# Optimization experiments

Hardware: AMD Instinct MI355X
Metric: run time of the kernel (lower is better)

Reference implementation:

```python
import jax, jax.numpy as jnp
import numpy as np

B, S = 16, 512
IN_DIM, ATTN_DIM, DEPTH, HEADS, DH = 512, 512, 4, 8, 64
CB_DIM, CB_SIZE, MAX_SEQ = 64, 8192, 544


def _ln(x, g, b):
    mu = x.mean(-1, keepdims=True)
    v = ((x - mu) ** 2).mean(-1, keepdims=True)
    return (x - mu) / jnp.sqrt(v + 1e-5) * g + b


def setup_inputs() -> dict:
    key = jax.random.key(0)
    ks = jax.random.split(key, 16)
    sc = 0.02
    d = {
        "x": jax.random.normal(ks[0], (B, S, IN_DIM), jnp.float32),
        "w_in": jax.random.normal(ks[1], (IN_DIM, ATTN_DIM), jnp.float32) * sc,
        "b_in": jnp.zeros((ATTN_DIM,), jnp.float32),
        "pos_emb": jax.random.normal(ks[2], (MAX_SEQ, ATTN_DIM), jnp.float32) * sc,
        "ln1_g": jnp.ones((DEPTH, ATTN_DIM), jnp.float32),
        "ln1_b": jnp.zeros((DEPTH, ATTN_DIM), jnp.float32),
        "wq": jax.random.normal(ks[3], (DEPTH, ATTN_DIM, ATTN_DIM), jnp.float32) * sc,
        "wk": jax.random.normal(ks[4], (DEPTH, ATTN_DIM, ATTN_DIM), jnp.float32) * sc,
        "wv": jax.random.normal(ks[5], (DEPTH, ATTN_DIM, ATTN_DIM), jnp.float32) * sc,
        "wo": jax.random.normal(ks[6], (DEPTH, ATTN_DIM, ATTN_DIM), jnp.float32) * sc,
        "ln2_g": jnp.ones((DEPTH, ATTN_DIM), jnp.float32),
        "ln2_b": jnp.zeros((DEPTH, ATTN_DIM), jnp.float32),
        "ff_w1": jax.random.normal(ks[7], (DEPTH, ATTN_DIM, 4 * ATTN_DIM), jnp.float32) * sc,
        "ff_b1": jnp.zeros((DEPTH, 4 * ATTN_DIM), jnp.float32),
        "ff_w2": jax.random.normal(ks[8], (DEPTH, 4 * ATTN_DIM, ATTN_DIM), jnp.float32) * sc,
        "ff_b2": jnp.zeros((DEPTH, ATTN_DIM), jnp.float32),
        "lnf_g": jnp.ones((ATTN_DIM,), jnp.float32),
        "lnf_b": jnp.zeros((ATTN_DIM,), jnp.float32),
        "w_out": jax.random.normal(ks[9], (ATTN_DIM, CB_DIM), jnp.float32) * sc,
        "b_out": jnp.zeros((CB_DIM,), jnp.float32),
        "codebook": jax.random.normal(ks[10], (CB_SIZE, CB_DIM), jnp.float32),
    }
    return d


def _attn(h, wq, wk, wv, wo):
    b, s, _ = h.shape
    q = jnp.einsum('bsd,de->bse', h, wq).reshape(b, s, HEADS, DH)
    k = jnp.einsum('bsd,de->bse', h, wk).reshape(b, s, HEADS, DH)
    v = jnp.einsum('bsd,de->bse', h, wv).reshape(b, s, HEADS, DH)
    scores = jnp.einsum('bqhd,bkhd->bhqk', q, k) * (DH ** -0.5)
    a = jax.nn.softmax(scores, axis=-1)
    o = jnp.einsum('bhqk,bkhd->bqhd', a, v).reshape(b, s, ATTN_DIM)
    return jnp.einsum('bse,ed->bsd', o, wo)


def reference(x, w_in, b_in, pos_emb, ln1_g, ln1_b, wq, wk, wv, wo,
              ln2_g, ln2_b, ff_w1, ff_b1, ff_w2, ff_b2, lnf_g, lnf_b,
              w_out, b_out, codebook):
    s = x.shape[1]
    # ContinuousTransformerWrapper: project in + absolute pos emb
    h = jnp.einsum('bsd,de->bse', x, w_in) + b_in + pos_emb[:s]
    # pre-norm encoder layers: attn + ff, each residual
    for i in range(DEPTH):
        h = h + _attn(_ln(h, ln1_g[i], ln1_b[i]), wq[i], wk[i], wv[i], wo[i])
        g = _ln(h, ln2_g[i], ln2_b[i])
        g = jax.nn.gelu(jnp.einsum('bsd,df->bsf', g, ff_w1[i]) + ff_b1[i])
        h = h + jnp.einsum('bsf,fd->bsd', g, ff_w2[i]) + ff_b2[i]
    h = _ln(h, lnf_g, lnf_b)
    z = jnp.einsum('bsd,dc->bsc', h, w_out) + b_out  # [B,S,CB_DIM]
    # VectorQuantize: euclidean nearest codebook entry
    d2 = (z ** 2).sum(-1, keepdims=True) - 2.0 * jnp.einsum('bsc,kc->bsk', z, codebook) \
         + (codebook ** 2).sum(-1)  # [B,S,CB_SIZE]
    idx = jnp.argmin(d2, axis=-1)
    q = codebook[idx]  # [B,S,CB_DIM]
    commit_loss = jnp.mean((jax.lax.stop_gradient(q) - z) ** 2)  # commitment_weight=1.0
    q_st = z + jax.lax.stop_gradient(q - z)  # straight-through
    return q_st.sum(axis=1), commit_loss
```

## Files before the change

kernel.cpp:

```cpp
#include <hip/hip_runtime.h>
#include <cmath>

#define BATCH 16
#define SEQ 512
#define DMODEL 512
#define NDEPTH 4
#define NHEADS 8
#define DHEAD 64
#define DFF 2048
#define CBD 64
#define CBS 8192
#define MROWS (BATCH * SEQ)

typedef unsigned short u16;
typedef __attribute__((ext_vector_type(8))) short short8;
typedef __attribute__((ext_vector_type(4))) float f32x4;
typedef __attribute__((ext_vector_type(4))) unsigned short u16x4;

__device__ __forceinline__ u16 f2bf(float f) {
    unsigned u = __float_as_uint(f);
    u += 0x7fff + ((u >> 16) & 1);
    return (u16)(u >> 16);
}
__device__ __forceinline__ float bf2f(u16 h) {
    return __uint_as_float(((unsigned)h) << 16);
}

__device__ __forceinline__ void async16(u16* lds, const u16* g) {
    __builtin_amdgcn_global_load_lds(
        (const __attribute__((address_space(1))) unsigned int*)g,
        (__attribute__((address_space(3))) unsigned int*)lds, 16, 0, 0);
}

__device__ __forceinline__ float gelu_tanh(float u) {
    float t = fmaf(0.07135481627f * u, u * u, 1.5957691216f * u);
    return u / (1.0f + __expf(-t));
}

__global__ void zero_kernel(float* __restrict__ p, int n) {
    int i = blockIdx.x * 256 + threadIdx.x;
    if (i < n) p[i] = 0.0f;
}

__global__ void cbn_kernel(const float* __restrict__ cb, float* __restrict__ cbn) {
    int c = blockIdx.x * 256 + threadIdx.x;
    if (c >= CBS) return;
    const float* row = cb + (size_t)c * CBD;
    float s = 0.0f;
#pragma unroll
    for (int d = 0; d < CBD; ++d) s += row[d] * row[d];
    cbn[c] = s;
}

__global__ __launch_bounds__(256) void wtrans_kernel(
    const float* __restrict__ W, u16* __restrict__ Th, u16* __restrict__ Tl,
    int K, int N, long inLS, long outLS) {
    __shared__ float t[32][33];
    const float* Ws = W + (size_t)blockIdx.z * inLS;
    u16* Tho = Th + (size_t)blockIdx.z * outLS;
    u16* Tlo = Tl + (size_t)blockIdx.z * outLS;
    int n0 = blockIdx.x * 32, k0 = blockIdx.y * 32;
    int tx = threadIdx.x & 31, ty = threadIdx.x >> 5;
#pragma unroll
    for (int r = ty; r < 32; r += 8) t[r][tx] = Ws[(size_t)(k0 + r) * N + n0 + tx];
    __syncthreads();
#pragma unroll
    for (int r = ty; r < 32; r += 8) {
        float v = t[tx][r];
        size_t o = (size_t)(n0 + r) * K + k0 + tx;
        u16 hh = f2bf(v);
        Tho[o] = hh;
        Tlo[o] = f2bf(v - bf2f(hh));
    }
}

__global__ __launch_bounds__(256) void vtrans_kernel(
    const u16* __restrict__ Qh, const u16* __restrict__ Ql,
    u16* __restrict__ VTh, u16* __restrict__ VTl) {
    __shared__ u16 t[64][68];
    int s0 = blockIdx.x * 64;
    int hh = blockIdx.y;
    int b = blockIdx.z & 15, plane = blockIdx.z >> 4;
    const u16* src = (plane ? Ql : Qh) + ((size_t)(16 + hh) * MROWS) * 64;
    u16* dst = (plane ? VTl : VTh);
    int tid = threadIdx.x;
    int rr = tid >> 4, c4 = (tid & 15) * 4;
#pragma unroll
    for (int i = 0; i < 4; ++i) {
        int r = rr + i * 16;
        const u16* p = src + (size_t)(b * SEQ + s0 + r) * 64 + c4;
        *(u16x4*)(&t[r][c4]) = *(const u16x4*)p;
    }
    __syncthreads();
#pragma unroll
    for (int i = 0; i < 4; ++i) {
        int r = rr + i * 16;
        u16x4 v;
        v.x = t[c4 + 0][r]; v.y = t[c4 + 1][r]; v.z = t[c4 + 2][r]; v.w = t[c4 + 3][r];
        *(u16x4*)(dst + (size_t)b * SEQ * DMODEL + (size_t)(hh * 64 + r) * SEQ + s0 + c4) = v;
    }
}

__global__ void split_kernel(const float* __restrict__ X, u16* __restrict__ H,
                             u16* __restrict__ L, int n) {
    int i = blockIdx.x * 256 + threadIdx.x;
    if (i < n) {
        float v = X[i];
        u16 hh = f2bf(v);
        H[i] = hh;
        L[i] = f2bf(v - bf2f(hh));
    }
}

__global__ __launch_bounds__(256) void ln_kernel(
    const float* __restrict__ X,
    const float* __restrict__ C0, const float* __restrict__ C1,
    const float* __restrict__ bias2, const float* __restrict__ pos2,
    float* __restrict__ Xout,
    float* __restrict__ Y, u16* __restrict__ Yh, u16* __restrict__ Yl,
    const float* __restrict__ g, const float* __restrict__ b) {
    int row  = blockIdx.x * 4 + (threadIdx.x >> 6);
    int lane = threadIdx.x & 63;
    float v[8];
    float s = 0.0f;
#pragma unroll
    for (int j = 0; j < 8; ++j) {
        int d = lane + j * 64;
        size_t o = (size_t)row * DMODEL + d;
        float t = X ? X[o] : 0.0f;
        if (C0)    t += C0[o] + C1[o];
        if (bias2) t += bias2[d];
        if (pos2)  t += pos2[(size_t)(row & (SEQ - 1)) * DMODEL + d];
        v[j] = t;
        if (Xout) Xout[o] = t;
        s += t;
    }
#pragma unroll
    for (int off = 32; off; off >>= 1) s += __shfl_xor(s, off);
    float mu  = s * (1.0f / DMODEL);
    float var = 0.0f;
#pragma unroll
    for (int j = 0; j < 8; ++j) { float d = v[j] - mu; var += d * d; }
#pragma unroll
    for (int off = 32; off; off >>= 1) var += __shfl_xor(var, off);
    float r = rsqrtf(var * (1.0f / DMODEL) + 1e-5f);
#pragma unroll
    for (int j = 0; j < 8; ++j) {
        int d = lane + j * 64;
        float y = (v[j] - mu) * r * g[d] + b[d];
        size_t o = (size_t)row * DMODEL + d;
        if (Y) Y[o] = y;
        if (Yh) {
            u16 hh = f2bf(y);
            Yh[o] = hh;
            Yl[o] = f2bf(y - bf2f(hh));
        }
    }
}

__global__ __launch_bounds__(256) void gemm3_kernel(
    const u16* __restrict__ Ah, const u16* __restrict__ Al,
    const u16* __restrict__ Bh, const u16* __restrict__ Bl,
    float* __restrict__ Cf, u16* __restrict__ Ch, u16* __restrict__ Cl,
    const float* __restrict__ bias, const float* __restrict__ res,
    const float* __restrict__ pos, int M, int N, int K, int gelu,
    float* __restrict__ Cs0, float* __restrict__ Cs1, int kslice, int qkvscatter) {
    __shared__ __align__(16) u16 AsH[128 * 64];
    __shared__ __align__(16) u16 AsL[128 * 64];
    __shared__ __align__(16) u16 BsH[128 * 64];
    __shared__ __align__(16) u16 BsL[128 * 64];

    int tid  = threadIdx.x;
    int w    = tid >> 6, lane = tid & 63;
    int wr   = w >> 1, wc = w & 1;
    int quad = lane >> 4, l16 = lane & 15;
    int m0   = blockIdx.x * 128;
    int n0   = blockIdx.y * 128;
    int ksA  = (kslice > 0) ? blockIdx.z * kslice : 0;
    int ksB  = (kslice > 0) ? ksA + kslice : K;

    f32x4 acc[4][4];
#pragma unroll
    for (int i = 0; i < 4; ++i)
#pragma unroll
        for (int j = 0; j < 4; ++j) acc[i][j] = (f32x4){0.f, 0.f, 0.f, 0.f};

    int ldsoff[4];
    size_t goff[4];
#pragma unroll
    for (int r = 0; r < 4; ++r) {
        int cidx = tid + 256 * r;
        int row = cidx >> 3;
        int cg = (cidx & 7) ^ (row & 7);
        ldsoff[r] = cidx * 8;
        goff[r] = (size_t)row * K + cg * 8;
    }

    const u16* AbaseH = Ah + (size_t)m0 * K;
    const u16* AbaseL = Al + (size_t)m0 * K;
    const u16* BbaseH = Bh + (size_t)n0 * K;
    const u16* BbaseL = Bl + (size_t)n0 * K;

    for (int ks = ksA; ks < ksB; ks += 64) {
        __syncthreads();
#pragma unroll
        for (int r = 0; r < 4; ++r) {
            size_t g = goff[r] + ks;
            async16(&AsH[ldsoff[r]], AbaseH + g);
            async16(&AsL[ldsoff[r]], AbaseL + g);
            async16(&BsH[ldsoff[r]], BbaseH + g);
            async16(&BsL[ldsoff[r]], BbaseL + g);
        }
        __syncthreads();
#pragma unroll
        for (int s = 0; s < 2; ++s) {
            short8 afh[4], afl[4];
#pragma unroll
            for (int i = 0; i < 4; ++i) {
                int row = wr * 64 + i * 16 + l16;
                int off = row * 64 + (((s << 2) | quad) ^ (row & 7)) * 8;
                afh[i] = *(const short8*)&AsH[off];
                afl[i] = *(const short8*)&AsL[off];
            }
#pragma unroll
            for (int j = 0; j < 4; ++j) {
                int rowb = wc * 64 + j * 16 + l16;
                int offb = rowb * 64 + (((s << 2) | quad) ^ (rowb & 7)) * 8;
                short8 bh = *(const short8*)&BsH[offb];
                short8 bl = *(const short8*)&BsL[offb];
#pragma unroll
                for (int i = 0; i < 4; ++i) {
                    acc[i][j] = __builtin_amdgcn_mfma_f32_16x16x32_bf16(afh[i], bh, acc[i][j], 0, 0, 0);
                    acc[i][j] = __builtin_amdgcn_mfma_f32_16x16x32_bf16(afl[i], bh, acc[i][j], 0, 0, 0);
                    acc[i][j] = __builtin_amdgcn_mfma_f32_16x16x32_bf16(afh[i], bl, acc[i][j], 0, 0, 0);
                }
            }
        }
    }

    float* Cspl = (kslice > 0) ? (blockIdx.z ? Cs1 : Cs0) : nullptr;
    int mbase = m0 + wr * 64;
    int nbase = n0 + wc * 64;
#pragma unroll
    for (int mi = 0; mi < 4; ++mi)
#pragma unroll
        for (int ni = 0; ni < 4; ++ni) {
            f32x4 a = acc[mi][ni];
#pragma unroll
            for (int r = 0; r < 4; ++r) {
                int m = mbase + mi * 16 + quad * 4 + r;
                int n = nbase + ni * 16 + l16;
                float v = a[r];
                size_t o = qkvscatter
                    ? ((size_t)(n >> 6) * M + m) * 64 + (n & 63)
                    : (size_t)m * N + n;
                if (Cspl) { Cspl[o] = v; continue; }
                if (bias) v += bias[n];
                if (pos)  v += pos[(size_t)(m & (SEQ - 1)) * N + n];
                if (res)  v += res[(size_t)m * N + n];
                if (gelu) v = gelu_tanh(v);
                if (Cf) Cf[o] = v;
                if (Ch) {
                    u16 hh = f2bf(v);
                    Ch[o] = hh;
                    Cl[o] = f2bf(v - bf2f(hh));
                }
            }
        }
}

__global__ __launch_bounds__(256) void gemm_kernel(
    const float* __restrict__ A, const float* __restrict__ Bm,
    float* __restrict__ C, const float* __restrict__ bias,
    int M, int N, int K) {
    __shared__ float As[16][68];
    __shared__ float Bs[16][64];
    int tid = threadIdx.x;
    int tx = tid & 15, ty = tid >> 4;
    int a_m = tid >> 2, a_k = (tid & 3) * 4;
    int b_k = tid >> 4, b_n = (tid & 15) * 4;
    const float* Arow = A + (size_t)(blockIdx.x * 64 + a_m) * K;
    const float* Bcol = Bm + (size_t)blockIdx.y * 64 + b_n;
    float acc[4][4] = {};
    for (int k0 = 0; k0 < K; k0 += 16) {
        float4 av = *(const float4*)(Arow + k0 + a_k);
        float4 bv = *(const float4*)(Bcol + (size_t)(k0 + b_k) * N);
        __syncthreads();
        As[a_k + 0][a_m] = av.x; As[a_k + 1][a_m] = av.y;
        As[a_k + 2][a_m] = av.z; As[a_k + 3][a_m] = av.w;
        *(float4*)(&Bs[b_k][b_n]) = bv;
        __syncthreads();
#pragma unroll
        for (int kk = 0; kk < 16; ++kk) {
            float4 a4 = *(const float4*)(&As[kk][ty * 4]);
            float4 b4 = *(const float4*)(&Bs[kk][tx * 4]);
            float ar[4] = {a4.x, a4.y, a4.z, a4.w};
            float br[4] = {b4.x, b4.y, b4.z, b4.w};
#pragma unroll
            for (int i = 0; i < 4; ++i)
#pragma unroll
                for (int j = 0; j < 4; ++j) acc[i][j] = fmaf(ar[i], br[j], acc[i][j]);
        }
    }
    int m0 = blockIdx.x * 64 + ty * 4;
    int n0 = blockIdx.y * 64 + tx * 4;
#pragma unroll
    for (int i = 0; i < 4; ++i) {
        float vv[4];
#pragma unroll
        for (int j = 0; j < 4; ++j) {
            float t = acc[i][j];
            if (bias) t += bias[n0 + j];
            vv[j] = t;
        }
        *(float4*)(C + (size_t)(m0 + i) * N + n0) = make_float4(vv[0], vv[1], vv[2], vv[3]);
    }
}

__global__ __launch_bounds__(256) void attn_flash_kernel(
    const u16* __restrict__ QKh, const u16* __restrict__ QKl,
    const u16* __restrict__ VTh, const u16* __restrict__ VTl,
    u16* __restrict__ Oh, u16* __restrict__ Ol) {
    int bh = blockIdx.x & 127;
    int qt = blockIdx.x >> 7;
    int bb = bh >> 3, hh = bh & 7;

    __shared__ __align__(16) float Pw[4][16 * 68];

    int tid = threadIdx.x;
    int w = tid >> 6, lane = tid & 63;
    int quad = lane >> 4, l16 = lane & 15;
    int qtile = qt * 4 + w;
    float* P = Pw[w];

    const u16* qrh = QKh + ((size_t)hh * MROWS + bb * SEQ + qtile * 16 + l16) * 64 + quad * 8;
    const u16* qrl = QKl + ((size_t)hh * MROWS + bb * SEQ + qtile * 16 + l16) * 64 + quad * 8;
    short8 Qh0 = *(const short8*)qrh;
    short8 Qh1 = *(const short8*)(qrh + 32);
    short8 Ql0 = *(const short8*)qrl;
    short8 Ql1 = *(const short8*)(qrl + 32);

    float lsum[4] = {0.f, 0.f, 0.f, 0.f};
    f32x4 acc[4];
#pragma unroll
    for (int dt = 0; dt < 4; ++dt) acc[dt] = (f32x4){0.f, 0.f, 0.f, 0.f};

    const u16* KbH = QKh + ((size_t)(8 + hh) * MROWS + bb * SEQ) * 64;
    const u16* KbL = QKl + ((size_t)(8 + hh) * MROWS + bb * SEQ) * 64;
    const u16* VbH = VTh + (size_t)bb * SEQ * DMODEL + (size_t)(hh * 64) * SEQ;
    const u16* VbL = VTl + (size_t)bb * SEQ * DMODEL + (size_t)(hh * 64) * SEQ;

    for (int kt = 0; kt < 8; ++kt) {
        int kb = kt * 64;
#pragma unroll
        for (int s = 0; s < 4; ++s) {
            const u16* kh = KbH + (size_t)(kb + s * 16 + l16) * 64 + quad * 8;
            const u16* kl = KbL + (size_t)(kb + s * 16 + l16) * 64 + quad * 8;
            f32x4 a = (f32x4){0.f, 0.f, 0.f, 0.f};
            {
                short8 Kh0 = *(const short8*)kh;
                short8 Kh1 = *(const short8*)(kh + 32);
                a = __builtin_amdgcn_mfma_f32_16x16x32_bf16(Qh0, Kh0, a, 0, 0, 0);
                a = __builtin_amdgcn_mfma_f32_16x16x32_bf16(Qh1, Kh1, a, 0, 0, 0);
                a = __builtin_amdgcn_mfma_f32_16x16x32_bf16(Ql0, Kh0, a, 0, 0, 0);
                a = __builtin_amdgcn_mfma_f32_16x16x32_bf16(Ql1, Kh1, a, 0, 0, 0);
            }
            {
                short8 Kl0 = *(const short8*)kl;
                short8 Kl1 = *(const short8*)(kl + 32);
                a = __builtin_amdgcn_mfma_f32_16x16x32_bf16(Qh0, Kl0, a, 0, 0, 0);
                a = __builtin_amdgcn_mfma_f32_16x16x32_bf16(Qh1, Kl1, a, 0, 0, 0);
            }
#pragma unroll
            for (int r = 0; r < 4; ++r) {
                float p = __expf(a[r] * 0.125f);
                lsum[r] += p;
                P[(quad * 4 + r) * 68 + s * 16 + l16] = p;
            }
        }
#pragma unroll
        for (int ks = 0; ks < 2; ++ks) {
            short8 ph, pl;
            {
                const float* src = &P[l16 * 68 + ks * 32 + quad * 8];
                f32x4 a0 = *(const f32x4*)src;
                f32x4 a1 = *(const f32x4*)(src + 4);
                float v[8] = {a0[0], a0[1], a0[2], a0[3], a1[0], a1[1], a1[2], a1[3]};
#pragma unroll
                for (int j = 0; j < 8; ++j) {
                    u16 hv = f2bf(v[j]);
                    ph[j] = (short)hv;
                    pl[j] = (short)f2bf(v[j] - bf2f(hv));
                }
            }
#pragma unroll
            for (int dt = 0; dt < 4; ++dt) {
                const u16* vh = VbH + (size_t)(dt * 16 + l16) * SEQ + kb + ks * 32 + quad * 8;
                const u16* vl = VbL + (size_t)(dt * 16 + l16) * SEQ + kb + ks * 32 + quad * 8;
                short8 Vh = *(const short8*)vh;
                short8 Vl = *(const short8*)vl;
                acc[dt] = __builtin_amdgcn_mfma_f32_16x16x32_bf16(ph, Vh, acc[dt], 0, 0, 0);
                acc[dt] = __builtin_amdgcn_mfma_f32_16x16x32_bf16(pl, Vh, acc[dt], 0, 0, 0);
                acc[dt] = __builtin_amdgcn_mfma_f32_16x16x32_bf16(ph, Vl, acc[dt], 0, 0, 0);
            }
        }
    }

#pragma unroll
    for (int r = 0; r < 4; ++r) {
#pragma unroll
        for (int off = 8; off; off >>= 1) lsum[r] += __shfl_xor(lsum[r], off);
    }
#pragma unroll
    for (int r = 0; r < 4; ++r) {
        float inv = 1.0f / lsum[r];
        size_t rowoff = (size_t)(bb * SEQ + qtile * 16 + quad * 4 + r) * DMODEL + hh * 64;
#pragma unroll
        for (int dt = 0; dt < 4; ++dt) {
            float v = acc[dt][r] * inv;
            u16 hv = f2bf(v);
            Oh[rowoff + dt * 16 + l16] = hv;
            Ol[rowoff + dt * 16 + l16] = f2bf(v - bf2f(hv));
        }
    }
}

__global__ __launch_bounds__(256) void vq3_kernel(
    const float* __restrict__ Z, const u16* __restrict__ Zh, const u16* __restrict__ Zl,
    const u16* __restrict__ CBh, const u16* __restrict__ CBl,
    const float* __restrict__ CB, const float* __restrict__ CBN,
    float* __restrict__ out) {
    __shared__ float sbest[4][16];
    __shared__ int sidx[4][16];
    __shared__ int ibest[16];
    __shared__ float psum[4][64];
    __shared__ float cl4[4];

    int tid = threadIdx.x;
    int w = tid >> 6, lane = tid & 63;
    int quad = lane >> 4, l16 = lane & 15;
    int row0 = blockIdx.x * 16;

    const u16* zph = Zh + (size_t)(row0 + l16) * CBD + quad * 8;
    const u16* zpl = Zl + (size_t)(row0 + l16) * CBD + quad * 8;
    short8 Z0h = *(const short8*)zph;
    short8 Z1h = *(const short8*)(zph + 32);
    short8 Z0l = *(const short8*)zpl;
    short8 Z1l = *(const short8*)(zpl + 32);

    float best[4] = {3.4e38f, 3.4e38f, 3.4e38f, 3.4e38f};
    int bidx[4] = {0, 0, 0, 0};

    short8 A0h, A1h, A0l, A1l;  float An;
    short8 B0h, B1h, B0l, B1l;  float Bn;
    short8 C0h, C1h, C0l, C1l;  float Cn;
    short8 D0h, D1h, D0l, D1l;  float Dn;

#define LOADB(bk, cc) {                                            \
    int c_ = (cc);                                                 \
    const u16* ph_ = CBh + (size_t)c_ * CBD + quad * 8;            \
    const u16* pl_ = CBl + (size_t)c_ * CBD + quad * 8;            \
    bk##0h = *(const short8*)ph_;  bk##1h = *(const short8*)(ph_ + 32); \
    bk##0l = *(const short8*)pl_;  bk##1l = *(const short8*)(pl_ + 32); \
    bk##n  = CBN[c_]; }

#define COMPB(bk, cc) {                                                          \
    f32x4 a_ = (f32x4){0.f, 0.f, 0.f, 0.f};                                      \
    int c_ = (cc);                                                               \
    a_ = __builtin_amdgcn_mfma_f32_16x16x32_bf16(Z0h, bk##0h, a_, 0, 0, 0);      \
    a_ = __builtin_amdgcn_mfma_f32_16x16x32_bf16(Z1h, bk##1h, a_, 0, 0, 0);      \
    a_ = __builtin_amdgcn_mfma_f32_16x16x32_bf16(Z0l, bk##0h, a_, 0, 0, 0);      \
    a_ = __builtin_amdgcn_mfma_f32_16x16x32_bf16(Z1l, bk##1h, a_, 0, 0, 0);      \
    a_ = __builtin_amdgcn_mfma_f32_16x16x32_bf16(Z0h, bk##0l, a_, 0, 0, 0);      \
    a_ = __builtin_amdgcn_mfma_f32_16x16x32_bf16(Z1h, bk##1l, a_, 0, 0, 0);      \
    _Pragma("unroll")                                                            \
    for (int r = 0; r < 4; ++r) {                                                \
        float s_ = bk##n - 2.0f * a_[r];                                         \
        if (s_ < best[r]) { best[r] = s_; bidx[r] = c_; }                        \
    } }

    const int NW = CBS / 4;
    int cbase = w * NW;
    LOADB(A, cbase + l16);
    LOADB(B, cbase + 16 + l16);
    LOADB(C, cbase + 32 + l16);
    LOADB(D, cbase + 48 + l16);
    for (int t = 0; t < NW; t += 64) {
        COMPB(A, cbase + t + l16);       LOADB(A, cbase + ((t + 64)  & (NW - 1)) + l16);
        COMPB(B, cbase + t + 16 + l16);  LOADB(B, cbase + ((t + 80)  & (NW - 1)) + l16);
        COMPB(C, cbase + t + 32 + l16);  LOADB(C, cbase + ((t + 96)  & (NW - 1)) + l16);
        COMPB(D, cbase + t + 48 + l16);  LOADB(D, cbase + ((t + 112) & (NW - 1)) + l16);
    }

#undef LOADB
#undef COMPB

#pragma unroll
    for (int off = 8; off; off >>= 1) {
#pragma unroll
        for (int r = 0; r < 4; ++r) {
            float ov = __shfl_xor(best[r], off);
            int oi = __shfl_xor(bidx[r], off);
            if (ov < best[r] || (ov == best[r] && oi < bidx[r])) { best[r] = ov; bidx[r] = oi; }
        }
    }
    if (l16 == 0) {
#pragma unroll
        for (int r = 0; r < 4; ++r) {
            sbest[w][quad * 4 + r] = best[r];
            sidx[w][quad * 4 + r] = bidx[r];
        }
    }
    __syncthreads();
    if (tid < 16) {
        float bv = sbest[0][tid];
        int bi = sidx[0][tid];
#pragma unroll
        for (int ww = 1; ww < 4; ++ww) {
            float ov = sbest[ww][tid];
            int oi = sidx[ww][tid];
            if (ov < bv || (ov == bv && oi < bi)) { bv = ov; bi = oi; }
        }
        ibest[tid] = bi;
    }
    __syncthreads();

    int d2 = lane;
    float qacc = 0.0f, closs = 0.0f;
#pragma unroll
    for (int j = 0; j < 4; ++j) {
        int r2 = w * 4 + j;
        int bi = ibest[r2];
        float q = CB[(size_t)bi * CBD + d2];
        float z = Z[(size_t)(row0 + r2) * CBD + d2];
        qacc += q;
        float df = q - z;
        closs += df * df;
    }
    psum[w][d2] = qacc;
#pragma unroll
    for (int off = 32; off; off >>= 1) closs += __shfl_xor(closs, off);
    if (d2 == 0) cl4[w] = closs;
    __syncthreads();
    if (tid < 64) {
        float t = psum[0][tid] + psum[1][tid] + psum[2][tid] + psum[3][tid];
        int b = row0 >> 9;
        atomicAdd(out + b * 64 + tid, t);
    }
    if (tid == 0)
        atomicAdd(out + 1024, (cl4[0] + cl4[1] + cl4[2] + cl4[3]) * (1.0f / (float)(MROWS * CBD)));
}

extern "C" void kernel_launch(void* const* d_in, const int* in_sizes, int n_in,
                              void* d_out, int out_size, void* d_ws, size_t ws_size,
                              hipStream_t stream) {
    const float* x    = (const float*)d_in[0];
    const float* w_in = (const float*)d_in[1];
    const float* b_in = (const float*)d_in[2];
    const float* pos  = (const float*)d_in[3];
    const float* ln1g = (const float*)d_in[4];
    const float* ln1b = (const float*)d_in[5];
    const float* wq   = (const float*)d_in[6];
    const float* wk   = (const float*)d_in[7];
    const float* wv   = (const float*)d_in[8];
    const float* wo   = (const float*)d_in[9];
    const float* ln2g = (const float*)d_in[10];
    const float* ln2b = (const float*)d_in[11];
    const float* ffw1 = (const float*)d_in[12];
    const float* ffb1 = (const float*)d_in[13];
    const float* ffw2 = (const float*)d_in[14];
    const float* ffb2 = (const float*)d_in[15];
    const float* lnfg = (const float*)d_in[16];
    const float* lnfb = (const float*)d_in[17];
    const float* wout = (const float*)d_in[18];
    const float* bout = (const float*)d_in[19];
    const float* cb   = (const float*)d_in[20];
    float* out = (float*)d_out;

    const size_t MD  = (size_t)MROWS * DMODEL;
    const size_t MQ  = (size_t)MROWS * 1536;
    const size_t MF  = (size_t)MROWS * DFF;

    float* ws   = (float*)d_ws;
    float* h    = ws;
    float* t0   = h + MD;
    float* big  = t0 + MD;
    float* zb   = big + MF;
    float* cbn  = zb + (size_t)MROWS * CBD;
    u16* cbh    = (u16*)(cbn + CBS);
    u16* cbl    = cbh + (size_t)CBS * CBD;
    u16* t0h    = (u16*)(cbh + 2 * (size_t)CBS * CBD);
    u16* t0l    = t0h + MD;
    u16* wb     = t0l + MD;

    u16* qkvh = (u16*)big;
    u16* qkvl = qkvh + MQ;
    u16* obh  = qkvl + MQ;
    u16* obl  = obh + MD;
    u16* xh   = obh;
    u16* xl   = obl;
    u16* fmh  = (u16*)big;
    u16* fml  = fmh + MF;
    u16* zbh  = (u16*)big;
    u16* zbl  = zbh + (size_t)MROWS * CBD;

    const size_t S_WIN  = (size_t)DMODEL * DMODEL;
    const size_t S_QKV  = (size_t)1536 * DMODEL * NDEPTH;
    const size_t S_WO   = S_WIN * NDEPTH;
    const size_t S_FF1  = (size_t)DFF * DMODEL * NDEPTH;
    const size_t S_FF2  = S_FF1;
    u16* winT_h = wb;
    u16* winT_l = winT_h + S_WIN;
    u16* qkvT_h = winT_l + S_WIN;
    u16* qkvT_l = qkvT_h + S_QKV;
    u16* woT_h  = qkvT_l + S_QKV;
    u16* woT_l  = woT_h + S_WO;
    u16* ff1T_h = woT_l + S_WO;
    u16* ff1T_l = ff1T_h + S_FF1;
    u16* ff2T_h = ff1T_l + S_FF1;
    u16* ff2T_l = ff2T_h + S_FF2;
    u16* VTh = ff2T_l + S_FF2;
    u16* VTl = VTh + (size_t)BATCH * SEQ * DMODEL;
    float* spK0 = (float*)(VTl + (size_t)BATCH * SEQ * DMODEL);
    float* spK1 = spK0 + MD;

    dim3 blk(256);

    zero_kernel<<<dim3((out_size + 255) / 256), blk, 0, stream>>>(out, out_size);
    cbn_kernel<<<dim3(CBS / 256), blk, 0, stream>>>(cb, cbn);
    split_kernel<<<dim3((int)(CBS * CBD / 256)), blk, 0, stream>>>(cb, cbh, cbl, CBS * CBD);

    wtrans_kernel<<<dim3(16, 16, 1), blk, 0, stream>>>(w_in, winT_h, winT_l, DMODEL, DMODEL, 0, 0);
    wtrans_kernel<<<dim3(16, 16, NDEPTH), blk, 0, stream>>>(
        wq, qkvT_h, qkvT_l, DMODEL, DMODEL, (long)DMODEL * DMODEL, (long)1536 * DMODEL);
    wtrans_kernel<<<dim3(16, 16, NDEPTH), blk, 0, stream>>>(
        wk, qkvT_h + (size_t)512 * DMODEL, qkvT_l + (size_t)512 * DMODEL,
        DMODEL, DMODEL, (long)DMODEL * DMODEL, (long)1536 * DMODEL);
    wtrans_kernel<<<dim3(16, 16, NDEPTH), blk, 0, stream>>>(
        wv, qkvT_h + (size_t)1024 * DMODEL, qkvT_l + (size_t)1024 * DMODEL,
        DMODEL, DMODEL, (long)DMODEL * DMODEL, (long)1536 * DMODEL);
    wtrans_kernel<<<dim3(16, 16, NDEPTH), blk, 0, stream>>>(
        wo, woT_h, woT_l, DMODEL, DMODEL, (long)DMODEL * DMODEL, (long)DMODEL * DMODEL);
    wtrans_kernel<<<dim3(DFF / 32, 16, NDEPTH), blk, 0, stream>>>(
        ffw1, ff1T_h, ff1T_l, DMODEL, DFF, (long)DMODEL * DFF, (long)DFF * DMODEL);
    wtrans_kernel<<<dim3(16, DFF / 32, NDEPTH), blk, 0, stream>>>(
        ffw2, ff2T_h, ff2T_l, DFF, DMODEL, (long)DFF * DMODEL, (long)DMODEL * DFF);

    split_kernel<<<dim3((int)(MD / 256)), blk, 0, stream>>>(x, xh, xl, (int)MD);

    gemm3_kernel<<<dim3(MROWS / 128, DMODEL / 128, 2), blk, 0, stream>>>(
        xh, xl, winT_h, winT_l, nullptr, nullptr, nullptr, nullptr, nullptr, nullptr,
        MROWS, DMODEL, DMODEL, 0, spK0, spK1, 256, 0);

    for (int l = 0; l < NDEPTH; ++l) {
        ln_kernel<<<dim3(MROWS / 4), blk, 0, stream>>>(
            (l == 0) ? nullptr : h, spK0, spK1,
            (l == 0) ? b_in : (ffb2 + (size_t)(l - 1) * DMODEL),
            (l == 0) ? pos : nullptr, h,
            nullptr, t0h, t0l, ln1g + l * DMODEL, ln1b + l * DMODEL);
        gemm3_kernel<<<dim3(MROWS / 128, 1536 / 128, 1), blk, 0, stream>>>(
            t0h, t0l, qkvT_h + (size_t)l * 1536 * DMODEL, qkvT_l + (size_t)l * 1536 * DMODEL,
            nullptr, qkvh, qkvl, nullptr, nullptr, nullptr, MROWS, 1536, DMODEL, 0,
            nullptr, nullptr, 0, 1);
        vtrans_kernel<<<dim3(8, 8, 32), blk, 0, stream>>>(qkvh, qkvl, VTh, VTl);
        attn_flash_kernel<<<dim3(1024), blk, 0, stream>>>(
            qkvh, qkvl, VTh, VTl, obh, obl);
        gemm3_kernel<<<dim3(MROWS / 128, DMODEL / 128, 2), blk, 0, stream>>>(
            obh, obl, woT_h + (size_t)l * S_WIN, woT_l + (size_t)l * S_WIN,
            nullptr, nullptr, nullptr, nullptr, nullptr, nullptr,
            MROWS, DMODEL, DMODEL, 0, spK0, spK1, 256, 0);
        ln_kernel<<<dim3(MROWS / 4), blk, 0, stream>>>(
            h, spK0, spK1, nullptr, nullptr, h,
            nullptr, t0h, t0l, ln2g + l * DMODEL, ln2b + l * DMODEL);
        gemm3_kernel<<<dim3(MROWS / 128, DFF / 128, 1), blk, 0, stream>>>(
            t0h, t0l, ff1T_h + (size_t)l * DFF * DMODEL, ff1T_l + (size_t)l * DFF * DMODEL,
            nullptr, fmh, fml, ffb1 + l * DFF, nullptr, nullptr, MROWS, DFF, DMODEL, 1,
            nullptr, nullptr, 0, 0);
        gemm3_kernel<<<dim3(MROWS / 128, DMODEL / 128, 2), blk, 0, stream>>>(
            fmh, fml, ff2T_h + (size_t)l * DFF * DMODEL, ff2T_l + (size_t)l * DFF * DMODEL,
            nullptr, nullptr, nullptr, nullptr, nullptr, nullptr,
            MROWS, DMODEL, DFF, 0, spK0, spK1, 1024, 0);
    }

    ln_kernel<<<dim3(MROWS / 4), blk, 0, stream>>>(
        h, spK0, spK1, ffb2 + (size_t)3 * DMODEL, nullptr, nullptr,
        t0, nullptr, nullptr, lnfg, lnfb);
    gemm_kernel<<<dim3(MROWS / 64, 1), blk, 0, stream>>>(t0, wout, zb, bout, MROWS, CBD, DMODEL);
    split_kernel<<<dim3((int)((size_t)MROWS * CBD / 256)), blk, 0, stream>>>(
        zb, zbh, zbl, MROWS * CBD);
    vq3_kernel<<<dim3(MROWS / 16), blk, 0, stream>>>(zb, zbh, zbl, cbh, cbl, cb, cbn, out);
}
```

Before: 1.811 ms.

## Stage K/V tiles in swizzled LDS shared across waves in flash attention

Each 64-key tile of K and V (high and low bf16 parts) is now loaded once per block into shared memory with async 16-byte copies, instead of every wave reading it straight from global memory. An XOR swizzle on 8-element chunks keeps LDS reads free of bank conflicts. The goal is to cut redundant global/L2 traffic, since the four waves of a block each reuse the same tile. In exchange, the loop is single-buffered with two block barriers per tile, so loads do not overlap compute, and LDS use per block grows by 32 KB.

```diff
diff --git a/kernel.cpp b/kernel.cpp
--- a/kernel.cpp
+++ b/kernel.cpp
@@ -326,6 +326,10 @@
     int bb = bh >> 3, hh = bh & 7;
 
     __shared__ __align__(16) float Pw[4][16 * 68];
+    __shared__ __align__(16) u16 KsH[64 * 64];
+    __shared__ __align__(16) u16 KsL[64 * 64];
+    __shared__ __align__(16) u16 VsH[64 * 64];
+    __shared__ __align__(16) u16 VsL[64 * 64];
 
     int tid = threadIdx.x;
     int w = tid >> 6, lane = tid & 63;
@@ -350,24 +354,48 @@
     const u16* VbH = VTh + (size_t)bb * SEQ * DMODEL + (size_t)(hh * 64) * SEQ;
     const u16* VbL = VTl + (size_t)bb * SEQ * DMODEL + (size_t)(hh * 64) * SEQ;
 
+    int ldsoff[2];
+    int goffK[2];
+    size_t goffV[2];
+#pragma unroll
+    for (int r = 0; r < 2; ++r) {
+        int cidx = tid + 256 * r;
+        int row = cidx >> 3;
+        int cg = (cidx & 7) ^ (row & 7);
+        ldsoff[r] = cidx * 8;
+        goffK[r] = row * 64 + cg * 8;
+        goffV[r] = (size_t)row * SEQ + cg * 8;
+    }
+
     for (int kt = 0; kt < 8; ++kt) {
         int kb = kt * 64;
+        __syncthreads();
+#pragma unroll
+        for (int r = 0; r < 2; ++r) {
+            async16(&KsH[ldsoff[r]], KbH + (size_t)kb * 64 + goffK[r]);
+            async16(&KsL[ldsoff[r]], KbL + (size_t)kb * 64 + goffK[r]);
+            async16(&VsH[ldsoff[r]], VbH + kb + goffV[r]);
+            async16(&VsL[ldsoff[r]], VbL + kb + goffV[r]);
+        }
+        __syncthreads();
+
 #pragma unroll
         for (int s = 0; s < 4; ++s) {
-            const u16* kh = KbH + (size_t)(kb + s * 16 + l16) * 64 + quad * 8;
-            const u16* kl = KbL + (size_t)(kb + s * 16 + l16) * 64 + quad * 8;
+            int row = s * 16 + l16;
+            int c0 = (quad ^ (row & 7)) * 8;
+            int c1 = ((quad | 4) ^ (row & 7)) * 8;
             f32x4 a = (f32x4){0.f, 0.f, 0.f, 0.f};
             {
-                short8 Kh0 = *(const short8*)kh;
-                short8 Kh1 = *(const short8*)(kh + 32);
+                short8 Kh0 = *(const short8*)&KsH[row * 64 + c0];
+                short8 Kh1 = *(const short8*)&KsH[row * 64 + c1];
                 a = __builtin_amdgcn_mfma_f32_16x16x32_bf16(Qh0, Kh0, a, 0, 0, 0);
                 a = __builtin_amdgcn_mfma_f32_16x16x32_bf16(Qh1, Kh1, a, 0, 0, 0);
                 a = __builtin_amdgcn_mfma_f32_16x16x32_bf16(Ql0, Kh0, a, 0, 0, 0);
                 a = __builtin_amdgcn_mfma_f32_16x16x32_bf16(Ql1, Kh1, a, 0, 0, 0);
             }
             {
-                short8 Kl0 = *(const short8*)kl;
-                short8 Kl1 = *(const short8*)(kl + 32);
+                short8 Kl0 = *(const short8*)&KsL[row * 64 + c0];
+                short8 Kl1 = *(const short8*)&KsL[row * 64 + c1];
                 a = __builtin_amdgcn_mfma_f32_16x16x32_bf16(Qh0, Kl0, a, 0, 0, 0);
                 a = __builtin_amdgcn_mfma_f32_16x16x32_bf16(Qh1, Kl1, a, 0, 0, 0);
             }
@@ -395,10 +423,10 @@
             }
 #pragma unroll
             for (int dt = 0; dt < 4; ++dt) {
-                const u16* vh = VbH + (size_t)(dt * 16 + l16) * SEQ + kb + ks * 32 + quad * 8;
-                const u16* vl = VbL + (size_t)(dt * 16 + l16) * SEQ + kb + ks * 32 + quad * 8;
-                short8 Vh = *(const short8*)vh;
-                short8 Vl = *(const short8*)vl;
+                int rowv = dt * 16 + l16;
+                int cv = (((ks << 2) | quad) ^ (rowv & 7)) * 8;
+                short8 Vh = *(const short8*)&VsH[rowv * 64 + cv];
+                short8 Vl = *(const short8*)&VsL[rowv * 64 + cv];
                 acc[dt] = __builtin_amdgcn_mfma_f32_16x16x32_bf16(ph, Vh, acc[dt], 0, 0, 0);
                 acc[dt] = __builtin_amdgcn_mfma_f32_16x16x32_bf16(pl, Vh, acc[dt], 0, 0, 0);
                 acc[dt] = __builtin_amdgcn_mfma_f32_16x16x32_bf16(ph, Vl, acc[dt], 0, 0, 0);
```

Measured after the change: 1.514 ms. 1.2x faster.
